# Performance work log

Hardware: AMD Instinct MI355X
Metric: run time of the kernel (lower is better)

Reference implementation:

```python
import jax, jax.numpy as jnp
import numpy as np
import math

D = 1024      # input/embed dim
H = 16        # heads
HD = D // H   # head dim
FF = 4096     # feedforward dim
B, S = 2, 2048
LN_EPS = 1e-5
NEG = -9e15


def setup_inputs() -> dict:
    key = jax.random.key(0)
    ks = jax.random.split(key, 16)
    inp = {
        "x": jax.random.normal(ks[0], (B, S, D), jnp.float32),
        "mask": jax.random.randint(ks[1], (1, 1, S, S), 0, 2, jnp.int32),
        "pos_bias": jax.random.normal(ks[2], (1, H, S, S), jnp.float32),
        "sinusoidal_pos": jax.random.normal(ks[3], (1, 1, S, HD), jnp.float32),
        # params (xavier-ish scale)
        "Wqkv": jax.random.normal(ks[4], (D, 3 * D), jnp.float32) * math.sqrt(2.0 / (D + 3 * D)),
        "bqkv": jnp.zeros((3 * D,), jnp.float32),
        "Wo": jax.random.normal(ks[5], (D, D), jnp.float32) * math.sqrt(1.0 / D),
        "bo": jnp.zeros((D,), jnp.float32),
        "W1": jax.random.normal(ks[6], (D, FF), jnp.float32) * math.sqrt(2.0 / (D + FF)),
        "b1": jnp.zeros((FF,), jnp.float32),
        "W2": jax.random.normal(ks[7], (FF, D), jnp.float32) * math.sqrt(2.0 / (D + FF)),
        "b2": jnp.zeros((D,), jnp.float32),
        "g1": jnp.ones((D,), jnp.float32),
        "be1": jnp.zeros((D,), jnp.float32),
        "g2": jnp.ones((D,), jnp.float32),
        "be2": jnp.zeros((D,), jnp.float32),
    }
    return inp


def _layernorm(x, g, b):
    mu = jnp.mean(x, axis=-1, keepdims=True)
    var = jnp.mean(jnp.square(x - mu), axis=-1, keepdims=True)
    return (x - mu) * jax.lax.rsqrt(var + LN_EPS) * g + b


def _rotate_half(x):
    # x: [..., HD] -> reshape [..., 2, HD//2], swap with negation, concat
    r = x.reshape(*x.shape[:-1], 2, -1)
    x1, x2 = r[..., 0, :], r[..., 1, :]
    return jnp.concatenate([-x2, x1], axis=-1)


def _rope(x, sp):
    # sp: [1,1,S,HD]; x: [B,H,S,HD]
    return x * jnp.cos(sp) + _rotate_half(x) * jnp.sin(sp)


def reference(x, mask, pos_bias, sinusoidal_pos, Wqkv, bqkv, Wo, bo,
              W1, b1, W2, b2, g1, be1, g2, be2):
    # pre-norm (note: residual uses the normalized x, matching the source)
    x = _layernorm(x, g1, be1)
    b, s, d = x.shape
    qkv = (x @ Wqkv + bqkv).reshape(b, s, H, 3 * HD).transpose(0, 2, 1, 3)
    q, k, v = jnp.split(qkv, 3, axis=-1)  # each [B,H,S,HD]
    sp = sinusoidal_pos[:, :, -s:]
    q = _rope(q, sp)
    k = _rope(k, sp)
    logits = jnp.einsum("bhqd,bhkd->bhqk", q, k)
    logits = (logits + pos_bias) / math.sqrt(HD)
    logits = jnp.where(mask == 0, NEG, logits)
    attn = jax.nn.softmax(logits, axis=-1)
    vals = jnp.einsum("bhqk,bhkd->bhqd", attn, v)
    vals = vals.transpose(0, 2, 1, 3).reshape(b, s, d)
    attn_out = vals @ Wo + bo
    x = x + attn_out
    x = _layernorm(x, g2, be2)
    h = jax.nn.gelu(x @ W1 + b1, approximate=False)  # torch GELU is exact
    x = x + (h @ W2 + b2)
    return x
```

## Files before the change

kernel.cpp:

```cpp
#include <hip/hip_runtime.h>
#include <math.h>

#define DD   1024
#define HH   16
#define HDD  64
#define FFF  4096
#define NB   2
#define NS   2048
#define NR   (NB * NS)
#define TDQ  (3 * DD)
#define NKT  (NS / 64)

typedef __attribute__((ext_vector_type(8))) _Float16 hfrag;
typedef __attribute__((ext_vector_type(4))) _Float16 h4v;
typedef __attribute__((ext_vector_type(16))) float f32x16;
typedef __attribute__((ext_vector_type(8))) unsigned short us8;
typedef __attribute__((ext_vector_type(4))) unsigned int u32x4;

__device__ __forceinline__ float4 ld4(const float* p) {
    return *reinterpret_cast<const float4*>(p);
}
__device__ __forceinline__ float gelu_f(float x) {
    return 0.5f * x * (1.0f + erff(x * 0.70710678118654752440f));
}
#define MFMA32H(a, b, c) __builtin_amdgcn_mfma_f32_32x32x16_f16((a), (b), (c), 0, 0, 0)

__global__ __launch_bounds__(256) void ln_kernel(const float* __restrict__ in,
        const float* __restrict__ gw, const float* __restrict__ bw,
        float* __restrict__ outf, _Float16* __restrict__ oh) {
    int row = blockIdx.x;
    float4 v = reinterpret_cast<const float4*>(in + (size_t)row * DD)[threadIdx.x];
    float s1 = v.x + v.y + v.z + v.w;
    float s2 = v.x * v.x + v.y * v.y + v.z * v.z + v.w * v.w;
#pragma unroll
    for (int off = 1; off < 64; off <<= 1) {
        s1 += __shfl_xor(s1, off);
        s2 += __shfl_xor(s2, off);
    }
    __shared__ float r1[4], r2[4];
    int wid = threadIdx.x >> 6;
    if ((threadIdx.x & 63) == 0) { r1[wid] = s1; r2[wid] = s2; }
    __syncthreads();
    s1 = r1[0] + r1[1] + r1[2] + r1[3];
    s2 = r2[0] + r2[1] + r2[2] + r2[3];
    float mu   = s1 * (1.0f / DD);
    float var  = s2 * (1.0f / DD) - mu * mu;
    float rstd = rsqrtf(var + 1e-5f);
    float4 g = reinterpret_cast<const float4*>(gw)[threadIdx.x];
    float4 b = reinterpret_cast<const float4*>(bw)[threadIdx.x];
    float o[4];
    o[0] = (v.x - mu) * rstd * g.x + b.x;
    o[1] = (v.y - mu) * rstd * g.y + b.y;
    o[2] = (v.z - mu) * rstd * g.z + b.z;
    o[3] = (v.w - mu) * rstd * g.w + b.w;
    float4 of; of.x = o[0]; of.y = o[1]; of.z = o[2]; of.w = o[3];
    reinterpret_cast<float4*>(outf + (size_t)row * DD)[threadIdx.x] = of;
    h4v hv;
#pragma unroll
    for (int j = 0; j < 4; ++j) hv[j] = (_Float16)o[j];
    *reinterpret_cast<h4v*>(oh + (size_t)row * DD + threadIdx.x * 4) = hv;
}

__global__ __launch_bounds__(256) void wt_convert(const float* __restrict__ W,
        _Float16* __restrict__ Th, int K, int N) {
    __shared__ float s[32][33];
    int tx = threadIdx.x & 31, ty = threadIdx.x >> 5;
    int n0 = blockIdx.x * 32, k0 = blockIdx.y * 32;
#pragma unroll
    for (int i = 0; i < 4; ++i)
        s[ty + i * 8][tx] = W[(size_t)(k0 + ty + i * 8) * N + n0 + tx];
    __syncthreads();
#pragma unroll
    for (int i = 0; i < 4; ++i) {
        int n = n0 + ty + i * 8;
        Th[(size_t)n * K + k0 + tx] = (_Float16)s[tx][ty + i * 8];
    }
}

__global__ __launch_bounds__(256) void cs_table(const float* __restrict__ sp,
        float* __restrict__ ct, float* __restrict__ st) {
    int i = blockIdx.x * 256 + threadIdx.x;
    float v = sp[i];
    ct[i] = cosf(v);
    st[i] = sinf(v);
}

__global__ __launch_bounds__(256) void mask8(const int* __restrict__ mask,
        unsigned char* __restrict__ mb) {
    int i = blockIdx.x * 256 + threadIdx.x;
    int4 v = reinterpret_cast<const int4*>(mask)[i];
    unsigned int o = (unsigned int)(v.x & 1) | ((unsigned int)(v.y & 1) << 8)
                   | ((unsigned int)(v.z & 1) << 16) | ((unsigned int)(v.w & 1) << 24);
    reinterpret_cast<unsigned int*>(mb)[i] = o;
}

__global__ __launch_bounds__(256) void rope_split(const _Float16* __restrict__ qkv,
        const float* __restrict__ ct, const float* __restrict__ st,
        _Float16* __restrict__ Qp, _Float16* __restrict__ Kp, _Float16* __restrict__ Vt) {
    __shared__ _Float16 sv[64][72];
    const int t = threadIdx.x;
    const int tile = blockIdx.x, bh = blockIdx.y;
    const int b = bh >> 4, h = bh & 15;
    const int r = t >> 2, p = t & 3;
    const int srow = tile * 64 + r;
    const _Float16* base = qkv + ((size_t)(b * NS + srow)) * TDQ + h * 192;

#pragma unroll
    for (int qk = 0; qk < 2; ++qk) {
        const _Float16* src = base + qk * 64;
        hfrag va = *reinterpret_cast<const hfrag*>(src + p * 8);
        hfrag vc = *reinterpret_cast<const hfrag*>(src + 32 + p * 8);
        hfrag o1, o2;
#pragma unroll
        for (int j = 0; j < 8; ++j) {
            int d1 = p * 8 + j, d2 = 32 + p * 8 + j;
            float a = (float)va[j], c = (float)vc[j];
            float c1 = ct[(size_t)srow * HDD + d1], s1 = st[(size_t)srow * HDD + d1];
            float c2 = ct[(size_t)srow * HDD + d2], s2 = st[(size_t)srow * HDD + d2];
            o1[j] = (_Float16)(a * c1 - c * s1);
            o2[j] = (_Float16)(c * c2 + a * s2);
        }
        _Float16* dst = qk ? Kp : Qp;
        size_t obase = ((size_t)bh * NS + srow) * HDD;
        *reinterpret_cast<hfrag*>(dst + obase + p * 8)      = o1;
        *reinterpret_cast<hfrag*>(dst + obase + 32 + p * 8) = o2;
    }
    const _Float16* vsrc = base + 128;
    hfrag v0 = *reinterpret_cast<const hfrag*>(vsrc + p * 16);
    hfrag v1 = *reinterpret_cast<const hfrag*>(vsrc + p * 16 + 8);
#pragma unroll
    for (int j = 0; j < 8; ++j) {
        sv[p * 16 + j][r]     = v0[j];
        sv[p * 16 + 8 + j][r] = v1[j];
    }
    __syncthreads();
    {
        int d = t >> 2, kb = (t & 3) * 16;
        size_t obase = ((size_t)bh * HDD + d) * NS + tile * 64 + kb;
        *reinterpret_cast<hfrag*>(Vt + obase)     = *reinterpret_cast<hfrag*>(&sv[d][kb]);
        *reinterpret_cast<hfrag*>(Vt + obase + 8) = *reinterpret_cast<hfrag*>(&sv[d][kb + 8]);
    }
}

__global__ __launch_bounds__(256) void attn_mfma(
        const _Float16* __restrict__ Qp, const _Float16* __restrict__ Kp,
        const _Float16* __restrict__ Vt,
        const float* __restrict__ pos_bias, const unsigned char* __restrict__ maskb,
        float* __restrict__ Opart, float2* __restrict__ Lpart) {
    __shared__ _Float16 kT[64][72];
    __shared__ _Float16 vT[64][72];
    __shared__ _Float16 PBs[4][32][68];
    const int t = threadIdx.x;
    const int w = t >> 6, lane = t & 63, lq = lane & 31, hi = lane >> 5;
    const int h = blockIdx.y >> 1, b = blockIdx.y & 1;
    const int bh = b * HH + h;
    const int qt = blockIdx.x, sp = blockIdx.z;
    const int q0 = qt * 128;
    const int qg = q0 + 32 * w + lq;
    const int sw = ((lq >> 3) & 3) << 3;
    const int KT0 = sp * 16, KT1 = KT0 + 16;
    const float C1  = 0.18033688011112042f;
    const float THR = 11.5f;

    hfrag qf[4];
#pragma unroll
    for (int dk = 0; dk < 4; ++dk)
        qf[dk] = *reinterpret_cast<const hfrag*>(
            Qp + ((size_t)bh * NS + qg) * HDD + 16 * dk + 8 * hi);

    f32x16 o0 = (f32x16)0.0f, o1 = (f32x16)0.0f;
    float mrun = -INFINITY, lsum = 0.0f;

    const int sr0 = t >> 2, sc = t & 3;
    const int swr = ((sr0 >> 3) & 3) << 3;
    const int brow = lane >> 4;
    const int bcol = (lane & 15) * 4;
    us8 kr[2], vr[2];
    float4 pbr[8]; unsigned int pmk[8];

#define STAGE_LOAD(KT) {                                                        \
        int kv0_ = (KT) * 64;                                                   \
        size_t kb_ = ((size_t)bh * NS + kv0_ + sr0) * HDD + 16 * sc;            \
        size_t vb_ = ((size_t)bh * HDD + sr0) * NS + kv0_ + 16 * sc;            \
        kr[0] = *reinterpret_cast<const us8*>(Kp + kb_);                        \
        kr[1] = *reinterpret_cast<const us8*>(Kp + kb_ + 8);                    \
        vr[0] = *reinterpret_cast<const us8*>(Vt + vb_);                        \
        vr[1] = *reinterpret_cast<const us8*>(Vt + vb_ + 8);                    \
        _Pragma("unroll")                                                       \
        for (int i = 0; i < 8; ++i) {                                           \
            int rg_ = q0 + 32 * w + brow + 4 * i;                               \
            pbr[i] = ld4(pos_bias + ((size_t)h * NS + rg_) * NS + kv0_ + bcol); \
            pmk[i] = *reinterpret_cast<const unsigned int*>(                    \
                         maskb + (size_t)rg_ * NS + kv0_ + bcol);               \
        }                                                                       \
    }

    STAGE_LOAD(KT0);
    for (int kt = KT0; kt < KT1; ++kt) {
        __syncthreads();
        *reinterpret_cast<us8*>(&kT[sr0][(16 * sc) ^ swr])     = kr[0];
        *reinterpret_cast<us8*>(&kT[sr0][(16 * sc + 8) ^ swr]) = kr[1];
        *reinterpret_cast<us8*>(&vT[sr0][(16 * sc) ^ swr])     = vr[0];
        *reinterpret_cast<us8*>(&vT[sr0][(16 * sc + 8) ^ swr]) = vr[1];
#pragma unroll
        for (int i = 0; i < 8; ++i) {
            h4v pv;
#pragma unroll
            for (int j = 0; j < 4; ++j)
                pv[j] = ((pmk[i] >> (8 * j)) & 0xffu)
                      ? (_Float16)(pbr[i][j] * C1) : (_Float16)(-60000.0f);
            *reinterpret_cast<h4v*>(&PBs[w][brow + 4 * i][bcol]) = pv;
        }
        __syncthreads();
        if (kt + 1 < KT1) STAGE_LOAD(kt + 1);

        f32x16 s0 = (f32x16)0.0f, s1 = (f32x16)0.0f;
#pragma unroll
        for (int dk = 0; dk < 4; ++dk) {
            hfrag k0 = *reinterpret_cast<const hfrag*>(&kT[lq][(16 * dk + 8 * hi) ^ sw]);
            hfrag k1 = *reinterpret_cast<const hfrag*>(&kT[32 + lq][(16 * dk + 8 * hi) ^ sw]);
            s0 = MFMA32H(k0, qf[dk], s0);
            s1 = MFMA32H(k1, qf[dk], s1);
        }
        float sv[2][16];
#pragma unroll
        for (int m2 = 0; m2 < 2; ++m2)
#pragma unroll
            for (int g = 0; g < 4; ++g) {
                h4v pb4 = *reinterpret_cast<const h4v*>(&PBs[w][lq][32 * m2 + 8 * g + 4 * hi]);
#pragma unroll
                for (int j = 0; j < 4; ++j) {
                    int r = 4 * g + j;
                    float sraw = (m2 == 0) ? s0[r] : s1[r];
                    sv[m2][r] = fmaf(sraw, C1, (float)pb4[j]);
                }
            }
        float mx = sv[0][0];
#pragma unroll
        for (int m2 = 0; m2 < 2; ++m2)
#pragma unroll
            for (int r = 0; r < 16; ++r) mx = fmaxf(mx, sv[m2][r]);
        mx = fmaxf(mx, __shfl_xor(mx, 32));
        if (__any(mx > mrun + THR)) {
            float mnew = fmaxf(mrun, mx);
            float corr = __builtin_amdgcn_exp2f(mrun - mnew);
            lsum *= corr;
            mrun = mnew;
#pragma unroll
            for (int r = 0; r < 16; ++r) {
                int iq = (r & 3) + 8 * (r >> 2) + 4 * hi;
                float cr = __shfl(corr, iq);
                o0[r] *= cr; o1[r] *= cr;
            }
        }
        float ps = 0.0f;
        hfrag af[4];
#pragma unroll
        for (int m2 = 0; m2 < 2; ++m2)
#pragma unroll
            for (int gp = 0; gp < 2; ++gp) {
                float p0 = __builtin_amdgcn_exp2f(sv[m2][8 * gp + 0] - mrun);
                float p1 = __builtin_amdgcn_exp2f(sv[m2][8 * gp + 1] - mrun);
                float p2 = __builtin_amdgcn_exp2f(sv[m2][8 * gp + 2] - mrun);
                float p3 = __builtin_amdgcn_exp2f(sv[m2][8 * gp + 3] - mrun);
                float p4 = __builtin_amdgcn_exp2f(sv[m2][8 * gp + 4] - mrun);
                float p5 = __builtin_amdgcn_exp2f(sv[m2][8 * gp + 5] - mrun);
                float p6 = __builtin_amdgcn_exp2f(sv[m2][8 * gp + 6] - mrun);
                float p7 = __builtin_amdgcn_exp2f(sv[m2][8 * gp + 7] - mrun);
                ps += (p0 + p1) + (p2 + p3) + (p4 + p5) + (p6 + p7);
                unsigned int XA = __builtin_bit_cast(unsigned int, __builtin_amdgcn_cvt_pkrtz(p0, p1));
                unsigned int XB = __builtin_bit_cast(unsigned int, __builtin_amdgcn_cvt_pkrtz(p2, p3));
                unsigned int XC = __builtin_bit_cast(unsigned int, __builtin_amdgcn_cvt_pkrtz(p4, p5));
                unsigned int XD = __builtin_bit_cast(unsigned int, __builtin_amdgcn_cvt_pkrtz(p6, p7));
                unsigned int YA = (unsigned int)__shfl_xor((int)XA, 32);
                unsigned int YB = (unsigned int)__shfl_xor((int)XB, 32);
                unsigned int YC = (unsigned int)__shfl_xor((int)XC, 32);
                unsigned int YD = (unsigned int)__shfl_xor((int)XD, 32);
                u32x4 aw;
                aw[0] = hi ? YC : XA;
                aw[1] = hi ? YD : XB;
                aw[2] = hi ? XC : YA;
                aw[3] = hi ? XD : YB;
                af[m2 * 2 + gp] = __builtin_bit_cast(hfrag, aw);
            }
        ps += __shfl_xor(ps, 32);
        lsum += ps;
#pragma unroll
        for (int kp = 0; kp < 4; ++kp) {
            hfrag v0 = *reinterpret_cast<const hfrag*>(&vT[lq][(16 * kp + 8 * hi) ^ sw]);
            hfrag v1 = *reinterpret_cast<const hfrag*>(&vT[32 + lq][(16 * kp + 8 * hi) ^ sw]);
            o0 = MFMA32H(af[kp], v0, o0);
            o1 = MFMA32H(af[kp], v1, o1);
        }
    }
#undef STAGE_LOAD
    size_t obase = (((size_t)(bh * 16 + qt)) * 2 + sp) * (size_t)(128 * 64);
#pragma unroll
    for (int r = 0; r < 16; ++r) {
        int iq = (r & 3) + 8 * (r >> 2) + 4 * hi;
        Opart[obase + (size_t)(32 * w + iq) * 64 + lq]      = o0[r];
        Opart[obase + (size_t)(32 * w + iq) * 64 + 32 + lq] = o1[r];
    }
    if (hi == 0) {
        float2 ml; ml.x = mrun; ml.y = lsum;
        Lpart[(((size_t)(bh * 16 + qt)) * 2 + sp) * 128 + 32 * w + lq] = ml;
    }
}

__global__ __launch_bounds__(256) void attn_combine(const float* __restrict__ Opart,
        const float2* __restrict__ Lpart, _Float16* __restrict__ valf) {
    const int qt = blockIdx.x;
    const int h = blockIdx.y >> 1, b = blockIdx.y & 1;
    const int bh = b * HH + h;
    const int t = threadIdx.x;
    const int qloc = t >> 2, d0 = (t & 3) * 16;
    size_t base = ((size_t)(bh * 16 + qt)) * 2;
#pragma unroll
    for (int half = 0; half < 2; ++half) {
        int q = qloc + 64 * half;
        float2 ml0 = Lpart[(base + 0) * 128 + q];
        float2 ml1 = Lpart[(base + 1) * 128 + q];
        float m = fmaxf(ml0.x, ml1.x);
        float a0 = __builtin_amdgcn_exp2f(ml0.x - m);
        float a1 = __builtin_amdgcn_exp2f(ml1.x - m);
        float inv = 1.0f / (ml0.y * a0 + ml1.y * a1);
        const float* O0 = Opart + (base + 0) * 8192 + (size_t)q * 64 + d0;
        const float* O1 = Opart + (base + 1) * 8192 + (size_t)q * 64 + d0;
        _Float16* dst = valf + ((size_t)(b * NS + qt * 128 + q)) * DD + h * HDD + d0;
#pragma unroll
        for (int j = 0; j < 4; ++j) {
            float4 x0 = ld4(O0 + 4 * j), x1 = ld4(O1 + 4 * j);
            h4v o;
            o[0] = (_Float16)((x0.x * a0 + x1.x * a1) * inv);
            o[1] = (_Float16)((x0.y * a0 + x1.y * a1) * inv);
            o[2] = (_Float16)((x0.z * a0 + x1.z * a1) * inv);
            o[3] = (_Float16)((x0.w * a0 + x1.w * a1) * inv);
            *reinterpret_cast<h4v*>(dst + 4 * j) = o;
        }
    }
}

template<int EPI>
__global__ __launch_bounds__(256, 2) void gemm_h(
        const _Float16* __restrict__ A, const _Float16* __restrict__ B,
        const float* __restrict__ bias, const float* __restrict__ resid,
        float* __restrict__ Cf, _Float16* __restrict__ Ch,
        int M, int N, int K) {
    __shared__ _Float16 sA[128][72];
    __shared__ _Float16 sB[128][72];
    const int t = threadIdx.x;
    const int w = t >> 6, lane = t & 63, lq = lane & 31, hi = lane >> 5;
    const int wr = w >> 1, wc = w & 1;
    const int m0 = blockIdx.y * 128, n0 = blockIdx.x * 128;
    const int sw = ((lq >> 3) & 3) << 3;

    f32x16 acc[2][2];
#pragma unroll
    for (int m = 0; m < 2; ++m)
#pragma unroll
        for (int n = 0; n < 2; ++n) acc[m][n] = (f32x16)0.0f;

    const int sr = t >> 1, skc = (t & 1) * 16;
    const int swr = ((sr >> 3) & 3) << 3;
    const _Float16* Ap = A + (size_t)(m0 + sr) * K + skc;
    const _Float16* Bp = B + (size_t)(n0 + sr) * K + skc;

    for (int k0 = 0; k0 < K; k0 += 32) {
        us8 a0 = *reinterpret_cast<const us8*>(Ap + k0);
        us8 a1 = *reinterpret_cast<const us8*>(Ap + k0 + 8);
        us8 b0 = *reinterpret_cast<const us8*>(Bp + k0);
        us8 b1 = *reinterpret_cast<const us8*>(Bp + k0 + 8);
        __syncthreads();
        *reinterpret_cast<us8*>(&sA[sr][(skc) ^ swr])     = a0;
        *reinterpret_cast<us8*>(&sA[sr][(skc + 8) ^ swr]) = a1;
        *reinterpret_cast<us8*>(&sB[sr][(skc) ^ swr])     = b0;
        *reinterpret_cast<us8*>(&sB[sr][(skc + 8) ^ swr]) = b1;
        __syncthreads();
        hfrag fa[2][2], fb[2][2];
#pragma unroll
        for (int mb = 0; mb < 2; ++mb)
#pragma unroll
            for (int kc = 0; kc < 2; ++kc)
                fa[mb][kc] = *reinterpret_cast<const hfrag*>(
                    &sA[wr * 64 + mb * 32 + lq][(kc * 16 + 8 * hi) ^ sw]);
#pragma unroll
        for (int nb = 0; nb < 2; ++nb)
#pragma unroll
            for (int kc = 0; kc < 2; ++kc)
                fb[nb][kc] = *reinterpret_cast<const hfrag*>(
                    &sB[wc * 64 + nb * 32 + lq][(kc * 16 + 8 * hi) ^ sw]);
#pragma unroll
        for (int kc = 0; kc < 2; ++kc)
#pragma unroll
            for (int mb = 0; mb < 2; ++mb)
#pragma unroll
                for (int nb = 0; nb < 2; ++nb)
                    acc[mb][nb] = MFMA32H(fa[mb][kc], fb[nb][kc], acc[mb][nb]);
    }
#pragma unroll
    for (int mb = 0; mb < 2; ++mb)
#pragma unroll
        for (int nb = 0; nb < 2; ++nb) {
            int colg = n0 + wc * 64 + nb * 32 + lq;
            float bv = bias[colg];
#pragma unroll
            for (int r = 0; r < 16; ++r) {
                int rowg = m0 + wr * 64 + mb * 32 + (r & 3) + 8 * (r >> 2) + 4 * hi;
                float v = acc[mb][nb][r] + bv;
                if (EPI == 1) v += resid[(size_t)rowg * N + colg];
                if (EPI == 2) {
                    Ch[(size_t)rowg * N + colg] = (_Float16)gelu_f(v);
                } else if (EPI == 3) {
                    Ch[(size_t)rowg * N + colg] = (_Float16)v;
                } else {
                    Cf[(size_t)rowg * N + colg] = v;
                }
            }
        }
}

__global__ __launch_bounds__(256, 2) void gemm_h2(
        const _Float16* __restrict__ A, const _Float16* __restrict__ B,
        const float* __restrict__ bias, const float* __restrict__ resid,
        float* __restrict__ Cf, int M, int N, int K) {
    __shared__ _Float16 sA[64][72];
    __shared__ _Float16 sB[128][72];
    const int t = threadIdx.x;
    const int w = t >> 6, lane = t & 63, lq = lane & 31, hi = lane >> 5;
    const int m0 = blockIdx.y * 64, n0 = blockIdx.x * 128;
    const int sw = ((lq >> 3) & 3) << 3;

    f32x16 acc[2];
    acc[0] = (f32x16)0.0f; acc[1] = (f32x16)0.0f;

    const int ar = t >> 2, akc = (t & 3) * 8;
    const int aswr = ((ar >> 3) & 3) << 3;
    const int br = t >> 1, bkc = (t & 1) * 16;
    const int bswr = ((br >> 3) & 3) << 3;
    const _Float16* Ap = A + (size_t)(m0 + ar) * K + akc;
    const _Float16* Bp = B + (size_t)(n0 + br) * K + bkc;

    for (int k0 = 0; k0 < K; k0 += 32) {
        us8 a0 = *reinterpret_cast<const us8*>(Ap + k0);
        us8 b0 = *reinterpret_cast<const us8*>(Bp + k0);
        us8 b1 = *reinterpret_cast<const us8*>(Bp + k0 + 8);
        __syncthreads();
        *reinterpret_cast<us8*>(&sA[ar][(akc) ^ aswr])     = a0;
        *reinterpret_cast<us8*>(&sB[br][(bkc) ^ bswr])     = b0;
        *reinterpret_cast<us8*>(&sB[br][(bkc + 8) ^ bswr]) = b1;
        __syncthreads();
        hfrag fa[2][2], fb[2];
#pragma unroll
        for (int mb = 0; mb < 2; ++mb)
#pragma unroll
            for (int kc = 0; kc < 2; ++kc)
                fa[mb][kc] = *reinterpret_cast<const hfrag*>(
                    &sA[mb * 32 + lq][(kc * 16 + 8 * hi) ^ sw]);
#pragma unroll
        for (int kc = 0; kc < 2; ++kc)
            fb[kc] = *reinterpret_cast<const hfrag*>(
                &sB[32 * w + lq][(kc * 16 + 8 * hi) ^ sw]);
#pragma unroll
        for (int kc = 0; kc < 2; ++kc)
#pragma unroll
            for (int mb = 0; mb < 2; ++mb)
                acc[mb] = MFMA32H(fa[mb][kc], fb[kc], acc[mb]);
    }
    int colg = n0 + 32 * w + lq;
    float bv = bias[colg];
#pragma unroll
    for (int mb = 0; mb < 2; ++mb)
#pragma unroll
        for (int r = 0; r < 16; ++r) {
            int rowg = m0 + mb * 32 + (r & 3) + 8 * (r >> 2) + 4 * hi;
            float v = acc[mb][r] + bv + resid[(size_t)rowg * N + colg];
            Cf[(size_t)rowg * N + colg] = v;
        }
}

extern "C" void kernel_launch(void* const* d_in, const int* in_sizes, int n_in,
                              void* d_out, int out_size, void* d_ws, size_t ws_size,
                              hipStream_t stream) {
    const float* x        = (const float*)d_in[0];
    const int*   mask     = (const int*)d_in[1];
    const float* pos_bias = (const float*)d_in[2];
    const float* sp       = (const float*)d_in[3];
    const float* Wqkv     = (const float*)d_in[4];
    const float* bqkv     = (const float*)d_in[5];
    const float* Wo       = (const float*)d_in[6];
    const float* bo       = (const float*)d_in[7];
    const float* W1       = (const float*)d_in[8];
    const float* b1       = (const float*)d_in[9];
    const float* W2       = (const float*)d_in[10];
    const float* b2       = (const float*)d_in[11];
    const float* g1       = (const float*)d_in[12];
    const float* be1      = (const float*)d_in[13];
    const float* g2       = (const float*)d_in[14];
    const float* be2      = (const float*)d_in[15];
    float* out = (float*)d_out;
    char* wsb = (char*)d_ws;

    float*          xbuf  = (float*)(wsb);
    _Float16*       actF  = (_Float16*)(wsb + ((size_t)16 << 20));
    _Float16*       wT    = (_Float16*)(wsb + ((size_t)24 << 20));
    float*          ct    = (float*)(wsb + ((size_t)32 << 20));
    float*          stb   = (float*)(wsb + ((size_t)33 << 20));
    unsigned char*  mkb   = (unsigned char*)(wsb + ((size_t)34 << 20));
    _Float16*       qkvh  = (_Float16*)(wsb + ((size_t)48 << 20));
    _Float16*       Qp    = (_Float16*)(wsb + ((size_t)72 << 20));
    _Float16*       Kp    = (_Float16*)(wsb + ((size_t)80 << 20));
    _Float16*       Vt    = (_Float16*)(wsb + ((size_t)88 << 20));
    _Float16*       hF    = (_Float16*)(wsb + ((size_t)48 << 20));
    float*          Opart = (float*)(wsb + ((size_t)96 << 20));
    float2*         Lpart = (float2*)(wsb + ((size_t)130 << 20));

    ln_kernel<<<NR, 256, 0, stream>>>(x, g1, be1, xbuf, actF);
    wt_convert<<<dim3(TDQ / 32, DD / 32), 256, 0, stream>>>(Wqkv, wT, DD, TDQ);
    gemm_h<3><<<dim3(TDQ / 128, NR / 128), 256, 0, stream>>>(
        actF, wT, bqkv, nullptr, nullptr, qkvh, NR, TDQ, DD);
    cs_table<<<(NS * HDD) / 256, 256, 0, stream>>>(sp, ct, stb);
    mask8<<<(NS * NS / 4) / 256, 256, 0, stream>>>(mask, mkb);
    rope_split<<<dim3(NS / 64, NB * HH), 256, 0, stream>>>(qkvh, ct, stb, Qp, Kp, Vt);
    attn_mfma<<<dim3(NS / 128, NB * HH, 2), 256, 0, stream>>>(
        Qp, Kp, Vt, pos_bias, mkb, Opart, Lpart);
    attn_combine<<<dim3(NS / 128, NB * HH), 256, 0, stream>>>(Opart, Lpart, actF);
    wt_convert<<<dim3(DD / 32, DD / 32), 256, 0, stream>>>(Wo, wT, DD, DD);
    gemm_h2<<<dim3(DD / 128, NR / 64), 256, 0, stream>>>(
        actF, wT, bo, xbuf, xbuf, NR, DD, DD);
    ln_kernel<<<NR, 256, 0, stream>>>(xbuf, g2, be2, xbuf, actF);
    wt_convert<<<dim3(FFF / 32, DD / 32), 256, 0, stream>>>(W1, wT, DD, FFF);
    gemm_h<2><<<dim3(FFF / 128, NR / 128), 256, 0, stream>>>(
        actF, wT, b1, nullptr, nullptr, hF, NR, FFF, DD);
    wt_convert<<<dim3(DD / 32, FFF / 32), 256, 0, stream>>>(W2, wT, FFF, DD);
    gemm_h2<<<dim3(DD / 128, NR / 64), 256, 0, stream>>>(
        hF, wT, b2, xbuf, out, NR, DD, FFF);
}
```

Before: 426.2 us.

## Process both batch elements per attention block to share pos_bias and mask loads

The attention kernel now handles both batch elements of a head in one block, so each pos_bias/mask tile is loaded and converted once and reused for the two batches. This halves the large fp32 pos_bias traffic, which is batch-independent. The cost is half as many blocks (256 instead of 512), doubled K/V shared memory, and more registers for duplicated accumulators and Q fragments, which may lower occupancy.

```diff
diff --git a/kernel.cpp b/kernel.cpp
--- a/kernel.cpp
+++ b/kernel.cpp
@@ -10,6 +10,7 @@
 #define NR   (NB * NS)
 #define TDQ  (3 * DD)
 #define NKT  (NS / 64)
+#define NSP  2
 
 typedef __attribute__((ext_vector_type(8))) _Float16 hfrag;
 typedef __attribute__((ext_vector_type(4))) _Float16 h4v;
@@ -147,45 +148,51 @@
         const _Float16* __restrict__ Vt,
         const float* __restrict__ pos_bias, const unsigned char* __restrict__ maskb,
         float* __restrict__ Opart, float2* __restrict__ Lpart) {
-    __shared__ _Float16 kT[64][72];
-    __shared__ _Float16 vT[64][72];
+    __shared__ _Float16 kT[2][64][72];
+    __shared__ _Float16 vT[2][64][72];
     __shared__ _Float16 PBs[4][32][68];
     const int t = threadIdx.x;
     const int w = t >> 6, lane = t & 63, lq = lane & 31, hi = lane >> 5;
-    const int h = blockIdx.y >> 1, b = blockIdx.y & 1;
-    const int bh = b * HH + h;
+    const int h = blockIdx.y;
     const int qt = blockIdx.x, sp = blockIdx.z;
     const int q0 = qt * 128;
     const int qg = q0 + 32 * w + lq;
     const int sw = ((lq >> 3) & 3) << 3;
-    const int KT0 = sp * 16, KT1 = KT0 + 16;
+    const int KT0 = sp * (NKT / NSP), KT1 = KT0 + (NKT / NSP);
     const float C1  = 0.18033688011112042f;
     const float THR = 11.5f;
 
-    hfrag qf[4];
-#pragma unroll
-    for (int dk = 0; dk < 4; ++dk)
-        qf[dk] = *reinterpret_cast<const hfrag*>(
-            Qp + ((size_t)bh * NS + qg) * HDD + 16 * dk + 8 * hi);
-
-    f32x16 o0 = (f32x16)0.0f, o1 = (f32x16)0.0f;
-    float mrun = -INFINITY, lsum = 0.0f;
+    hfrag qf[2][4];
+#pragma unroll
+    for (int bt = 0; bt < 2; ++bt)
+#pragma unroll
+        for (int dk = 0; dk < 4; ++dk)
+            qf[bt][dk] = *reinterpret_cast<const hfrag*>(
+                Qp + ((size_t)(bt * HH + h) * NS + qg) * HDD + 16 * dk + 8 * hi);
+
+    f32x16 o[2][2];
+#pragma unroll
+    for (int bt = 0; bt < 2; ++bt) { o[bt][0] = (f32x16)0.0f; o[bt][1] = (f32x16)0.0f; }
+    float mrun[2] = { -INFINITY, -INFINITY }, lsum[2] = { 0.0f, 0.0f };
 
     const int sr0 = t >> 2, sc = t & 3;
     const int swr = ((sr0 >> 3) & 3) << 3;
     const int brow = lane >> 4;
     const int bcol = (lane & 15) * 4;
-    us8 kr[2], vr[2];
+    us8 kr[2][2], vr[2][2];
     float4 pbr[8]; unsigned int pmk[8];
 
 #define STAGE_LOAD(KT) {                                                        \
         int kv0_ = (KT) * 64;                                                   \
-        size_t kb_ = ((size_t)bh * NS + kv0_ + sr0) * HDD + 16 * sc;            \
-        size_t vb_ = ((size_t)bh * HDD + sr0) * NS + kv0_ + 16 * sc;            \
-        kr[0] = *reinterpret_cast<const us8*>(Kp + kb_);                        \
-        kr[1] = *reinterpret_cast<const us8*>(Kp + kb_ + 8);                    \
-        vr[0] = *reinterpret_cast<const us8*>(Vt + vb_);                        \
-        vr[1] = *reinterpret_cast<const us8*>(Vt + vb_ + 8);                    \
+        _Pragma("unroll")                                                       \
+        for (int bt = 0; bt < 2; ++bt) {                                        \
+            size_t kb_ = ((size_t)(bt * HH + h) * NS + kv0_ + sr0) * HDD + 16 * sc; \
+            size_t vb_ = ((size_t)(bt * HH + h) * HDD + sr0) * NS + kv0_ + 16 * sc; \
+            kr[bt][0] = *reinterpret_cast<const us8*>(Kp + kb_);                \
+            kr[bt][1] = *reinterpret_cast<const us8*>(Kp + kb_ + 8);            \
+            vr[bt][0] = *reinterpret_cast<const us8*>(Vt + vb_);                \
+            vr[bt][1] = *reinterpret_cast<const us8*>(Vt + vb_ + 8);            \
+        }                                                                       \
         _Pragma("unroll")                                                       \
         for (int i = 0; i < 8; ++i) {                                           \
             int rg_ = q0 + 32 * w + brow + 4 * i;                               \
@@ -198,10 +205,13 @@
     STAGE_LOAD(KT0);
     for (int kt = KT0; kt < KT1; ++kt) {
         __syncthreads();
-        *reinterpret_cast<us8*>(&kT[sr0][(16 * sc) ^ swr])     = kr[0];
-        *reinterpret_cast<us8*>(&kT[sr0][(16 * sc + 8) ^ swr]) = kr[1];
-        *reinterpret_cast<us8*>(&vT[sr0][(16 * sc) ^ swr])     = vr[0];
-        *reinterpret_cast<us8*>(&vT[sr0][(16 * sc + 8) ^ swr]) = vr[1];
+#pragma unroll
+        for (int bt = 0; bt < 2; ++bt) {
+            *reinterpret_cast<us8*>(&kT[bt][sr0][(16 * sc) ^ swr])     = kr[bt][0];
+            *reinterpret_cast<us8*>(&kT[bt][sr0][(16 * sc + 8) ^ swr]) = kr[bt][1];
+            *reinterpret_cast<us8*>(&vT[bt][sr0][(16 * sc) ^ swr])     = vr[bt][0];
+            *reinterpret_cast<us8*>(&vT[bt][sr0][(16 * sc + 8) ^ swr]) = vr[bt][1];
+        }
 #pragma unroll
         for (int i = 0; i < 8; ++i) {
             h4v pv;
@@ -214,96 +224,107 @@
         __syncthreads();
         if (kt + 1 < KT1) STAGE_LOAD(kt + 1);
 
-        f32x16 s0 = (f32x16)0.0f, s1 = (f32x16)0.0f;
-#pragma unroll
-        for (int dk = 0; dk < 4; ++dk) {
-            hfrag k0 = *reinterpret_cast<const hfrag*>(&kT[lq][(16 * dk + 8 * hi) ^ sw]);
-            hfrag k1 = *reinterpret_cast<const hfrag*>(&kT[32 + lq][(16 * dk + 8 * hi) ^ sw]);
-            s0 = MFMA32H(k0, qf[dk], s0);
-            s1 = MFMA32H(k1, qf[dk], s1);
-        }
-        float sv[2][16];
-#pragma unroll
-        for (int m2 = 0; m2 < 2; ++m2)
-#pragma unroll
-            for (int g = 0; g < 4; ++g) {
-                h4v pb4 = *reinterpret_cast<const h4v*>(&PBs[w][lq][32 * m2 + 8 * g + 4 * hi]);
-#pragma unroll
-                for (int j = 0; j < 4; ++j) {
-                    int r = 4 * g + j;
-                    float sraw = (m2 == 0) ? s0[r] : s1[r];
-                    sv[m2][r] = fmaf(sraw, C1, (float)pb4[j]);
+#pragma unroll
+        for (int bt = 0; bt < 2; ++bt) {
+            f32x16 s0 = (f32x16)0.0f, s1 = (f32x16)0.0f;
+#pragma unroll
+            for (int dk = 0; dk < 4; ++dk) {
+                hfrag k0 = *reinterpret_cast<const hfrag*>(
+                    &kT[bt][lq][(16 * dk + 8 * hi) ^ sw]);
+                hfrag k1 = *reinterpret_cast<const hfrag*>(
+                    &kT[bt][32 + lq][(16 * dk + 8 * hi) ^ sw]);
+                s0 = MFMA32H(k0, qf[bt][dk], s0);
+                s1 = MFMA32H(k1, qf[bt][dk], s1);
+            }
+            float sv[2][16];
+#pragma unroll
+            for (int m2 = 0; m2 < 2; ++m2)
+#pragma unroll
+                for (int g = 0; g < 4; ++g) {
+                    h4v pb4 = *reinterpret_cast<const h4v*>(
+                        &PBs[w][lq][32 * m2 + 8 * g + 4 * hi]);
+#pragma unroll
+                    for (int j = 0; j < 4; ++j) {
+                        int r = 4 * g + j;
+                        float sraw = (m2 == 0) ? s0[r] : s1[r];
+                        sv[m2][r] = fmaf(sraw, C1, (float)pb4[j]);
+                    }
+                }
+            float mx = sv[0][0];
+#pragma unroll
+            for (int m2 = 0; m2 < 2; ++m2)
+#pragma unroll
+                for (int r = 0; r < 16; ++r) mx = fmaxf(mx, sv[m2][r]);
+            mx = fmaxf(mx, __shfl_xor(mx, 32));
+            if (__any(mx > mrun[bt] + THR)) {
+                float mnew = fmaxf(mrun[bt], mx);
+                float corr = __builtin_amdgcn_exp2f(mrun[bt] - mnew);
+                lsum[bt] *= corr;
+                mrun[bt] = mnew;
+#pragma unroll
+                for (int r = 0; r < 16; ++r) {
+                    int iq = (r & 3) + 8 * (r >> 2) + 4 * hi;
+                    float cr = __shfl(corr, iq);
+                    o[bt][0][r] *= cr; o[bt][1][r] *= cr;
                 }
             }
-        float mx = sv[0][0];
-#pragma unroll
-        for (int m2 = 0; m2 < 2; ++m2)
-#pragma unroll
-            for (int r = 0; r < 16; ++r) mx = fmaxf(mx, sv[m2][r]);
-        mx = fmaxf(mx, __shfl_xor(mx, 32));
-        if (__any(mx > mrun + THR)) {
-            float mnew = fmaxf(mrun, mx);
-            float corr = __builtin_amdgcn_exp2f(mrun - mnew);
-            lsum *= corr;
-            mrun = mnew;
-#pragma unroll
-            for (int r = 0; r < 16; ++r) {
-                int iq = (r & 3) + 8 * (r >> 2) + 4 * hi;
-                float cr = __shfl(corr, iq);
-                o0[r] *= cr; o1[r] *= cr;
+            float ps = 0.0f;
+            hfrag af[4];
+#pragma unroll
+            for (int m2 = 0; m2 < 2; ++m2)
+#pragma unroll
+                for (int gp = 0; gp < 2; ++gp) {
+                    float p0 = __builtin_amdgcn_exp2f(sv[m2][8 * gp + 0] - mrun[bt]);
+                    float p1 = __builtin_amdgcn_exp2f(sv[m2][8 * gp + 1] - mrun[bt]);
+                    float p2 = __builtin_amdgcn_exp2f(sv[m2][8 * gp + 2] - mrun[bt]);
+                    float p3 = __builtin_amdgcn_exp2f(sv[m2][8 * gp + 3] - mrun[bt]);
+                    float p4 = __builtin_amdgcn_exp2f(sv[m2][8 * gp + 4] - mrun[bt]);
+                    float p5 = __builtin_amdgcn_exp2f(sv[m2][8 * gp + 5] - mrun[bt]);
+                    float p6 = __builtin_amdgcn_exp2f(sv[m2][8 * gp + 6] - mrun[bt]);
+                    float p7 = __builtin_amdgcn_exp2f(sv[m2][8 * gp + 7] - mrun[bt]);
+                    ps += (p0 + p1) + (p2 + p3) + (p4 + p5) + (p6 + p7);
+                    unsigned int XA = __builtin_bit_cast(unsigned int, __builtin_amdgcn_cvt_pkrtz(p0, p1));
+                    unsigned int XB = __builtin_bit_cast(unsigned int, __builtin_amdgcn_cvt_pkrtz(p2, p3));
+                    unsigned int XC = __builtin_bit_cast(unsigned int, __builtin_amdgcn_cvt_pkrtz(p4, p5));
+                    unsigned int XD = __builtin_bit_cast(unsigned int, __builtin_amdgcn_cvt_pkrtz(p6, p7));
+                    unsigned int YA = (unsigned int)__shfl_xor((int)XA, 32);
+                    unsigned int YB = (unsigned int)__shfl_xor((int)XB, 32);
+                    unsigned int YC = (unsigned int)__shfl_xor((int)XC, 32);
+                    unsigned int YD = (unsigned int)__shfl_xor((int)XD, 32);
+                    u32x4 aw;
+                    aw[0] = hi ? YC : XA;
+                    aw[1] = hi ? YD : XB;
+                    aw[2] = hi ? XC : YA;
+                    aw[3] = hi ? XD : YB;
+                    af[m2 * 2 + gp] = __builtin_bit_cast(hfrag, aw);
+                }
+            ps += __shfl_xor(ps, 32);
+            lsum[bt] += ps;
+#pragma unroll
+            for (int kp = 0; kp < 4; ++kp) {
+                hfrag v0 = *reinterpret_cast<const hfrag*>(
+                    &vT[bt][lq][(16 * kp + 8 * hi) ^ sw]);
+                hfrag v1 = *reinterpret_cast<const hfrag*>(
+                    &vT[bt][32 + lq][(16 * kp + 8 * hi) ^ sw]);
+                o[bt][0] = MFMA32H(af[kp], v0, o[bt][0]);
+                o[bt][1] = MFMA32H(af[kp], v1, o[bt][1]);
             }
         }
-        float ps = 0.0f;
-        hfrag af[4];
-#pragma unroll
-        for (int m2 = 0; m2 < 2; ++m2)
-#pragma unroll
-            for (int gp = 0; gp < 2; ++gp) {
-                float p0 = __builtin_amdgcn_exp2f(sv[m2][8 * gp + 0] - mrun);
-                float p1 = __builtin_amdgcn_exp2f(sv[m2][8 * gp + 1] - mrun);
-                float p2 = __builtin_amdgcn_exp2f(sv[m2][8 * gp + 2] - mrun);
-                float p3 = __builtin_amdgcn_exp2f(sv[m2][8 * gp + 3] - mrun);
-                float p4 = __builtin_amdgcn_exp2f(sv[m2][8 * gp + 4] - mrun);
-                float p5 = __builtin_amdgcn_exp2f(sv[m2][8 * gp + 5] - mrun);
-                float p6 = __builtin_amdgcn_exp2f(sv[m2][8 * gp + 6] - mrun);
-                float p7 = __builtin_amdgcn_exp2f(sv[m2][8 * gp + 7] - mrun);
-                ps += (p0 + p1) + (p2 + p3) + (p4 + p5) + (p6 + p7);
-                unsigned int XA = __builtin_bit_cast(unsigned int, __builtin_amdgcn_cvt_pkrtz(p0, p1));
-                unsigned int XB = __builtin_bit_cast(unsigned int, __builtin_amdgcn_cvt_pkrtz(p2, p3));
-                unsigned int XC = __builtin_bit_cast(unsigned int, __builtin_amdgcn_cvt_pkrtz(p4, p5));
-                unsigned int XD = __builtin_bit_cast(unsigned int, __builtin_amdgcn_cvt_pkrtz(p6, p7));
-                unsigned int YA = (unsigned int)__shfl_xor((int)XA, 32);
-                unsigned int YB = (unsigned int)__shfl_xor((int)XB, 32);
-                unsigned int YC = (unsigned int)__shfl_xor((int)XC, 32);
-                unsigned int YD = (unsigned int)__shfl_xor((int)XD, 32);
-                u32x4 aw;
-                aw[0] = hi ? YC : XA;
-                aw[1] = hi ? YD : XB;
-                aw[2] = hi ? XC : YA;
-                aw[3] = hi ? XD : YB;
-                af[m2 * 2 + gp] = __builtin_bit_cast(hfrag, aw);
-            }
-        ps += __shfl_xor(ps, 32);
-        lsum += ps;
-#pragma unroll
-        for (int kp = 0; kp < 4; ++kp) {
-            hfrag v0 = *reinterpret_cast<const hfrag*>(&vT[lq][(16 * kp + 8 * hi) ^ sw]);
-            hfrag v1 = *reinterpret_cast<const hfrag*>(&vT[32 + lq][(16 * kp + 8 * hi) ^ sw]);
-            o0 = MFMA32H(af[kp], v0, o0);
-            o1 = MFMA32H(af[kp], v1, o1);
-        }
     }
 #undef STAGE_LOAD
-    size_t obase = (((size_t)(bh * 16 + qt)) * 2 + sp) * (size_t)(128 * 64);
-#pragma unroll
-    for (int r = 0; r < 16; ++r) {
-        int iq = (r & 3) + 8 * (r >> 2) + 4 * hi;
-        Opart[obase + (size_t)(32 * w + iq) * 64 + lq]      = o0[r];
-        Opart[obase + (size_t)(32 * w + iq) * 64 + 32 + lq] = o1[r];
-    }
-    if (hi == 0) {
-        float2 ml; ml.x = mrun; ml.y = lsum;
-        Lpart[(((size_t)(bh * 16 + qt)) * 2 + sp) * 128 + 32 * w + lq] = ml;
+#pragma unroll
+    for (int bt = 0; bt < 2; ++bt) {
+        size_t obase = (((size_t)((bt * HH + h) * 16 + qt)) * NSP + sp) * (size_t)(128 * 64);
+#pragma unroll
+        for (int r = 0; r < 16; ++r) {
+            int iq = (r & 3) + 8 * (r >> 2) + 4 * hi;
+            Opart[obase + (size_t)(32 * w + iq) * 64 + lq]      = o[bt][0][r];
+            Opart[obase + (size_t)(32 * w + iq) * 64 + 32 + lq] = o[bt][1][r];
+        }
+        if (hi == 0) {
+            float2 ml; ml.x = mrun[bt]; ml.y = lsum[bt];
+            Lpart[(((size_t)((bt * HH + h) * 16 + qt)) * NSP + sp) * 128 + 32 * w + lq] = ml;
+        }
     }
 }
 
@@ -314,7 +335,7 @@
     const int bh = b * HH + h;
     const int t = threadIdx.x;
     const int qloc = t >> 2, d0 = (t & 3) * 16;
-    size_t base = ((size_t)(bh * 16 + qt)) * 2;
+    size_t base = ((size_t)(bh * 16 + qt)) * NSP;
 #pragma unroll
     for (int half = 0; half < 2; ++half) {
         int q = qloc + 64 * half;
@@ -521,7 +542,7 @@
     cs_table<<<(NS * HDD) / 256, 256, 0, stream>>>(sp, ct, stb);
     mask8<<<(NS * NS / 4) / 256, 256, 0, stream>>>(mask, mkb);
     rope_split<<<dim3(NS / 64, NB * HH), 256, 0, stream>>>(qkvh, ct, stb, Qp, Kp, Vt);
-    attn_mfma<<<dim3(NS / 128, NB * HH, 2), 256, 0, stream>>>(
+    attn_mfma<<<dim3(NS / 128, HH, NSP), 256, 0, stream>>>(
         Qp, Kp, Vt, pos_bias, mkb, Opart, Lpart);
     attn_combine<<<dim3(NS / 128, NB * HH), 256, 0, stream>>>(Opart, Lpart, actF);
     wt_convert<<<dim3(DD / 32, DD / 32), 256, 0, stream>>>(Wo, wT, DD, DD);
```

After: 406.2 us. -4.7%, faster.
